# Kernel optimization log

Measured on AMD Instinct MI355X. Metric: run time of the kernel, lower is better.

Reference implementation:

```python
import jax, jax.numpy as jnp
import numpy as np

N_SPACE = 197  # spatial tokens (ViT-B/16: 196 patches + CLS)
T = 8          # frames, fixed by space_time_pos shape (197*8, dim)
H = 12         # heads


def setup_inputs() -> dict:
    key = jax.random.key(0)
    ks = jax.random.split(key, 8)
    dim = 768
    B = 8
    Nq = 1576
    scale = dim ** -0.5
    return {
        "s_x": jax.random.normal(ks[0], (N_SPACE, B * T, dim), jnp.float32),
        "t_x": jax.random.normal(ks[1], (B, Nq, dim), jnp.float32),
        "space_time_pos": scale * jax.random.normal(ks[2], (N_SPACE * T, dim), jnp.float32),
        "q_w": jax.random.normal(ks[3], (dim, dim), jnp.float32) * 0.02,
        "q_b": jnp.zeros((dim,), jnp.float32),
        "kv_w": jax.random.normal(ks[4], (2 * dim, dim), jnp.float32) * 0.02,
        "kv_b": jnp.zeros((2 * dim,), jnp.float32),
        "proj_w": jax.random.normal(ks[5], (dim, dim), jnp.float32) * 0.02,
        "proj_b": jnp.zeros((dim,), jnp.float32),
    }


def reference(s_x, t_x, space_time_pos, q_w, q_b, kv_w, kv_b, proj_w, proj_b):
    n, BT, dim = s_x.shape
    B, Nq, _ = t_x.shape
    t = BT // B
    head_dim = dim // H
    scale = head_dim ** -0.5

    # rearrange 'n (b t) d -> b (t n) d'
    s = s_x.reshape(n, B, t, dim).transpose(1, 2, 0, 3).reshape(B, t * n, dim)
    s = s + space_time_pos  # (B, t*n, dim)

    # Q from t_x, K/V from s
    q = t_x @ q_w.T + q_b                      # (B, Nq, dim)
    kv = s @ kv_w.T + kv_b                     # (B, t*n, 2*dim)
    Nk = t * n
    # 'b n (e h d) -> e b h n d'
    kv = kv.reshape(B, Nk, 2, H, head_dim).transpose(2, 0, 3, 1, 4)
    k, v = kv[0], kv[1]                        # (B, H, Nk, hd)
    q = q.reshape(B, Nq, H, head_dim).transpose(0, 2, 1, 3) * scale  # (B, H, Nq, hd)

    attn = jnp.einsum('bhqd,bhkd->bhqk', q, k)
    attn = jax.nn.softmax(attn, axis=-1)
    out = jnp.einsum('bhqk,bhkd->bhqd', attn, v)   # (B, H, Nq, hd)
    out = out.transpose(0, 2, 1, 3).reshape(B, Nq, dim)
    return out @ proj_w.T + proj_b
```

## Files before the change

kernel.cpp:

```cpp
#include <hip/hip_runtime.h>
#include <stdint.h>

#define NSPACE 197
#define TFRAMES 8
#define NH 12
#define DIM 768
#define HD 64
#define BATCH 8
#define NQ 1576
#define NK 1576
#define M_REAL 12608
#define M_PAD 12672
#define VT_LD 1600

typedef __attribute__((ext_vector_type(8))) short s16x8;
typedef __attribute__((ext_vector_type(4))) short s16x4;
typedef __attribute__((ext_vector_type(4))) float f32x4;

__device__ inline uint16_t f2bf(float f) {
    union { float f; uint32_t i; } c; c.f = f;
    uint32_t r = c.i + 0x7FFF + ((c.i >> 16) & 1);
    return (uint16_t)(r >> 16);
}
__device__ inline uint32_t pack2bf(float lo, float hi) {
    union { float f; uint32_t i; } a, b; a.f = lo; b.f = hi;
    return ((a.i + 0x8000u) >> 16) | ((b.i + 0x8000u) & 0xFFFF0000u);
}


__global__ void conv_f2b(const float* __restrict__ src, uint16_t* __restrict__ dst, int n8) {
    int chunk = blockIdx.x * 256 + threadIdx.x;
    if (chunk >= n8) return;
    size_t off = (size_t)chunk * 8;
    float4 a = *(const float4*)(src + off);
    float4 b = *(const float4*)(src + off + 4);
    s16x8 o;
    o[0] = (short)f2bf(a.x); o[1] = (short)f2bf(a.y);
    o[2] = (short)f2bf(a.z); o[3] = (short)f2bf(a.w);
    o[4] = (short)f2bf(b.x); o[5] = (short)f2bf(b.y);
    o[6] = (short)f2bf(b.z); o[7] = (short)f2bf(b.w);
    *(s16x8*)(dst + off) = o;
}

__global__ void fill_x(const float* __restrict__ t_x, uint16_t* __restrict__ x_pad) {
    int chunk = blockIdx.x * 256 + threadIdx.x;
    const int total = M_PAD * (DIM / 8);
    if (chunk >= total) return;
    size_t off = (size_t)chunk * 8;
    s16x8 o;
    if (off < (size_t)M_REAL * DIM) {
        float4 a = *(const float4*)(t_x + off);
        float4 b = *(const float4*)(t_x + off + 4);
        o[0] = (short)f2bf(a.x); o[1] = (short)f2bf(a.y);
        o[2] = (short)f2bf(a.z); o[3] = (short)f2bf(a.w);
        o[4] = (short)f2bf(b.x); o[5] = (short)f2bf(b.y);
        o[6] = (short)f2bf(b.z); o[7] = (short)f2bf(b.w);
    } else {
        for (int j = 0; j < 8; j++) o[j] = 0;
    }
    *(s16x8*)(x_pad + off) = o;
}

__global__ void fill_s(const float* __restrict__ s_x, const float* __restrict__ pos,
                       uint16_t* __restrict__ s_pad) {
    int chunk = blockIdx.x * 256 + threadIdx.x;
    const int total = M_PAD * (DIM / 8);
    if (chunk >= total) return;
    int i = chunk / (DIM / 8);
    int cc = chunk - i * (DIM / 8);
    int d0 = cc * 8;
    uint16_t* dst = s_pad + (size_t)i * DIM + d0;
    if (i >= M_REAL) {
        s16x8 z; for (int j = 0; j < 8; j++) z[j] = 0;
        *(s16x8*)dst = z;
        return;
    }
    int b = i / NK, rr = i - b * NK;
    int t_i = rr / NSPACE, n_i = rr - t_i * NSPACE;
    const float* src = s_x + ((size_t)(n_i * (BATCH * TFRAMES) + b * TFRAMES + t_i)) * DIM + d0;
    const float* ps = pos + (size_t)rr * DIM + d0;
    float4 a0 = *(const float4*)src;
    float4 a1 = *(const float4*)(src + 4);
    float4 p0 = *(const float4*)ps;
    float4 p1 = *(const float4*)(ps + 4);
    s16x8 o;
    o[0] = (short)f2bf(a0.x + p0.x); o[1] = (short)f2bf(a0.y + p0.y);
    o[2] = (short)f2bf(a0.z + p0.z); o[3] = (short)f2bf(a0.w + p0.w);
    o[4] = (short)f2bf(a1.x + p1.x); o[5] = (short)f2bf(a1.y + p1.y);
    o[6] = (short)f2bf(a1.z + p1.z); o[7] = (short)f2bf(a1.w + p1.w);
    *(s16x8*)dst = o;
}

template <int MODE>
__global__ __launch_bounds__(256)
void gemm_bt(const uint16_t* __restrict__ A, const uint16_t* __restrict__ W,
             const float* __restrict__ bias,
             uint16_t* __restrict__ out0, uint16_t* __restrict__ out1,
             float* __restrict__ outf) {
    __shared__ uint16_t As[128 * 40];
    __shared__ uint16_t Bs[128 * 40];
    const int t = threadIdx.x;
    const int lane = t & 63, w = t >> 6;
    const int r16 = lane & 15, quad = lane >> 4;
    const int wm = w >> 1, wn = w & 1;
    const int m0 = blockIdx.y * 128;
    const int n0 = blockIdx.x * 128;

    f32x4 acc[4][4];
    for (int a = 0; a < 4; a++)
        for (int bb = 0; bb < 4; bb++)
            for (int r = 0; r < 4; r++) acc[a][bb][r] = 0.f;

    for (int kk = 0; kk < DIM; kk += 32) {
        for (int i2 = 0; i2 < 2; i2++) {
            int c = t + i2 * 256;
            int row = c >> 2, kc = (c & 3) * 8;
            *(s16x8*)&As[row * 40 + kc] = *(const s16x8*)&A[(size_t)(m0 + row) * DIM + kk + kc];
            *(s16x8*)&Bs[row * 40 + kc] = *(const s16x8*)&W[(size_t)(n0 + row) * DIM + kk + kc];
        }
        __syncthreads();
        s16x8 af[4], bfr[4];
        for (int mt = 0; mt < 4; mt++)
            af[mt] = *(const s16x8*)&As[(wm * 64 + mt * 16 + r16) * 40 + quad * 8];
        for (int nt = 0; nt < 4; nt++)
            bfr[nt] = *(const s16x8*)&Bs[(wn * 64 + nt * 16 + r16) * 40 + quad * 8];
        for (int mt = 0; mt < 4; mt++)
            for (int nt = 0; nt < 4; nt++)
                acc[mt][nt] = __builtin_amdgcn_mfma_f32_16x16x32_bf16(af[mt], bfr[nt], acc[mt][nt], 0, 0, 0);
        __syncthreads();
    }

    for (int mt = 0; mt < 4; mt++)
        for (int nt = 0; nt < 4; nt++) {
            int col = n0 + wn * 64 + nt * 16 + r16;
            float bz = bias[col];
            int rowb = m0 + wm * 64 + mt * 16 + quad * 4;
            for (int r = 0; r < 4; r++) {
                int i = rowb + r;
                if (i >= M_REAL) continue;
                float v = acc[mt][nt][r] + bz;
                if (MODE == 0) {
                    int b = i / NQ, nq = i - b * NQ;
                    int h = col >> 6, d = col & 63;
                    out0[(size_t)(((b * NH + h) * NQ) + nq) * HD + d] = f2bf(v * 0.18033688011112042f);
                } else if (MODE == 1) {
                    int b = i / NK, nk = i - b * NK;
                    if (col < DIM) {
                        int h = col >> 6, d = col & 63;
                        out0[(size_t)(((b * NH + h) * NK) + nk) * HD + d] = f2bf(v);
                    } else {
                        int c2 = col - DIM;
                        int h = c2 >> 6, d = c2 & 63;
                        out1[(size_t)(((b * NH + h) * NK) + nk) * HD + d] = f2bf(v);
                    }
                } else {
                    outf[(size_t)i * DIM + col] = v;
                }
            }
        }
}

__global__ __launch_bounds__(256)
void transpose_v(const uint16_t* __restrict__ v, uint16_t* __restrict__ vt) {
    __shared__ uint16_t T[64 * 72];
    int tile = blockIdx.x, bh = blockIdx.y;
    int nk0 = tile * 64;
    const uint16_t* V = v + (size_t)bh * NK * HD;
    uint16_t* VT = vt + (size_t)bh * HD * VT_LD;
    int tid = threadIdx.x;
    int rr = tid >> 3;
    int c8 = (tid & 7) * 8;
    for (int p = 0; p < 2; p++) {
        int lr = p * 32 + rr;
        int nk = nk0 + lr;
        s16x8 val;
        if (nk < NK) val = *(const s16x8*)(V + (size_t)nk * HD + c8);
        else for (int j = 0; j < 8; j++) val[j] = 0;
        for (int j = 0; j < 8; j++)
            T[(c8 + j) * 72 + lr] = (uint16_t)val[j];
    }
    __syncthreads();
    for (int p = 0; p < 2; p++) {
        int d = p * 32 + rr;
        s16x8 o = *(const s16x8*)&T[d * 72 + c8];
        *(s16x8*)(VT + (size_t)d * VT_LD + nk0 + c8) = o;
    }
}

#define NITER 50
__global__ __launch_bounds__(256)
void flash_attn(const uint16_t* __restrict__ q_buf, const uint16_t* __restrict__ k_buf,
                const uint16_t* __restrict__ vt_buf, uint16_t* __restrict__ ao) {
    __shared__ uint16_t Kb[2][32 * 72];
    __shared__ uint16_t Vb[2][64 * 40];
    int h = blockIdx.y, b = blockIdx.z;
    int tid = threadIdx.x;
    int lane = tid & 63, w = tid >> 6;
    int r16 = lane & 15, quad = lane >> 4;
    size_t bh = (size_t)(b * NH + h);
    const uint16_t* Q = q_buf + bh * NQ * HD;
    const uint16_t* K = k_buf + bh * NK * HD;
    const uint16_t* VT = vt_buf + bh * HD * VT_LD;
    int q0 = blockIdx.x * 128 + w * 32;

    const int kg = tid >> 3;
    const int kc = (tid & 7) * 8;
    const int kslot = ((kg >> 3) << 2) + (kg & 3) + ((kg & 4) ? 16 : 0);
    const int vd = tid >> 2;
    const int vc = (tid & 3) * 8;
    const uint16_t* Kg = K + (size_t)kg * HD + kc;
    const uint16_t* Vg = VT + (size_t)vd * VT_LD + vc;
    uint16_t* Kw = &Kb[0][kslot * 72 + kc];
    uint16_t* Vw = &Vb[0][vd * 40 + vc];
    const int KBSZ = 32 * 72, VBSZ = 64 * 40;

    s16x8 qf[2][2];
    for (int m = 0; m < 2; m++) {
        int qrow = q0 + m * 16 + r16;
        if (qrow < NQ) {
            qf[m][0] = *(const s16x8*)(Q + (size_t)qrow * HD + quad * 8);
            qf[m][1] = *(const s16x8*)(Q + (size_t)qrow * HD + 32 + quad * 8);
        } else {
            for (int j = 0; j < 8; j++) { qf[m][0][j] = 0; qf[m][1][j] = 0; }
        }
    }

    f32x4 oT[2][4];
    f32x4 lsum4[2];
    for (int m = 0; m < 2; m++) {
        for (int dt = 0; dt < 4; dt++)
            for (int r = 0; r < 4; r++) oT[m][dt][r] = 0.f;
        for (int r = 0; r < 4; r++) lsum4[m][r] = 0.f;
    }

    {
        s16x8 kv = *(const s16x8*)Kg;
        s16x8 vv = *(const s16x8*)Vg;
        *(s16x8*)Kw = kv;
        *(s16x8*)Vw = vv;
    }
    __syncthreads();

    for (int it = 0; it < NITER; it++) {
        int kb = it * 32;
        int cur = it & 1, nxt = cur ^ 1;
        s16x8 knv, vnv;
        bool have_next = (it + 1 < NITER);
        if (have_next) {
            knv = *(const s16x8*)(Kg + (size_t)(kb + 32) * HD);
            vnv = *(const s16x8*)(Vg + kb + 32);
        }

        const uint16_t* Kc = &Kb[cur][0];
        const uint16_t* Vc = &Vb[cur][0];
        s16x8 kfA0 = *(const s16x8*)(Kc + r16 * 72 + quad * 8);
        s16x8 kfA1 = *(const s16x8*)(Kc + r16 * 72 + 32 + quad * 8);
        s16x8 kfB0 = *(const s16x8*)(Kc + (16 + r16) * 72 + quad * 8);
        s16x8 kfB1 = *(const s16x8*)(Kc + (16 + r16) * 72 + 32 + quad * 8);

        s16x8 pf[2];
        if (it < NITER - 1) {
            #pragma unroll
            for (int m = 0; m < 2; m++) {
                f32x4 sA, sB;
                for (int r = 0; r < 4; r++) { sA[r] = 0.f; sB[r] = 0.f; }
                sA = __builtin_amdgcn_mfma_f32_16x16x32_bf16(kfA0, qf[m][0], sA, 0, 0, 0);
                sA = __builtin_amdgcn_mfma_f32_16x16x32_bf16(kfA1, qf[m][1], sA, 0, 0, 0);
                sB = __builtin_amdgcn_mfma_f32_16x16x32_bf16(kfB0, qf[m][0], sB, 0, 0, 0);
                sB = __builtin_amdgcn_mfma_f32_16x16x32_bf16(kfB1, qf[m][1], sB, 0, 0, 0);
                f32x4 pA, pB;
                #pragma unroll
                for (int r = 0; r < 4; r++) { pA[r] = exp2f(sA[r]); pB[r] = exp2f(sB[r]); }
                lsum4[m] += pA;
                lsum4[m] += pB;
                union { s16x8 v; uint32_t u[4]; } pk;
                pk.u[0] = pack2bf(pA[0], pA[1]);
                pk.u[1] = pack2bf(pA[2], pA[3]);
                pk.u[2] = pack2bf(pB[0], pB[1]);
                pk.u[3] = pack2bf(pB[2], pB[3]);
                pf[m] = pk.v;
            }
        } else {
            #pragma unroll
            for (int m = 0; m < 2; m++) {
                f32x4 sA, sB;
                for (int r = 0; r < 4; r++) { sA[r] = 0.f; sB[r] = 0.f; }
                sA = __builtin_amdgcn_mfma_f32_16x16x32_bf16(kfA0, qf[m][0], sA, 0, 0, 0);
                sA = __builtin_amdgcn_mfma_f32_16x16x32_bf16(kfA1, qf[m][1], sA, 0, 0, 0);
                sB = __builtin_amdgcn_mfma_f32_16x16x32_bf16(kfB0, qf[m][0], sB, 0, 0, 0);
                sB = __builtin_amdgcn_mfma_f32_16x16x32_bf16(kfB1, qf[m][1], sB, 0, 0, 0);
                f32x4 pA, pB;
                #pragma unroll
                for (int r = 0; r < 4; r++) {
                    pA[r] = (kb + quad * 8 + r < NK)     ? exp2f(sA[r]) : 0.f;
                    pB[r] = (kb + quad * 8 + 4 + r < NK) ? exp2f(sB[r]) : 0.f;
                }
                lsum4[m] += pA;
                lsum4[m] += pB;
                union { s16x8 v; uint32_t u[4]; } pk;
                pk.u[0] = pack2bf(pA[0], pA[1]);
                pk.u[1] = pack2bf(pA[2], pA[3]);
                pk.u[2] = pack2bf(pB[0], pB[1]);
                pk.u[3] = pack2bf(pB[2], pB[3]);
                pf[m] = pk.v;
            }
        }
        #pragma unroll
        for (int dt = 0; dt < 4; dt++) {
            s16x8 vf = *(const s16x8*)(Vc + (dt * 16 + r16) * 40 + quad * 8);
            oT[0][dt] = __builtin_amdgcn_mfma_f32_16x16x32_bf16(vf, pf[0], oT[0][dt], 0, 0, 0);
            oT[1][dt] = __builtin_amdgcn_mfma_f32_16x16x32_bf16(vf, pf[1], oT[1][dt], 0, 0, 0);
        }
        if (have_next) {
            *(s16x8*)(Kw + nxt * KBSZ) = knv;
            *(s16x8*)(Vw + nxt * VBSZ) = vnv;
        }
        __syncthreads();
    }

    #pragma unroll
    for (int m = 0; m < 2; m++) {
        float rs = lsum4[m][0] + lsum4[m][1] + lsum4[m][2] + lsum4[m][3];
        rs += __shfl_xor(rs, 16);
        rs += __shfl_xor(rs, 32);
        int q = q0 + m * 16 + r16;
        if (q >= NQ) continue;
        float inv = 1.0f / rs;
        size_t rowoff = (size_t)(b * NQ + q) * DIM + h * HD;
        #pragma unroll
        for (int dt = 0; dt < 4; dt++) {
            s16x4 o4;
            o4[0] = (short)f2bf(oT[m][dt][0] * inv);
            o4[1] = (short)f2bf(oT[m][dt][1] * inv);
            o4[2] = (short)f2bf(oT[m][dt][2] * inv);
            o4[3] = (short)f2bf(oT[m][dt][3] * inv);
            *(s16x4*)(ao + rowoff + dt * 16 + quad * 4) = o4;
        }
    }
}

extern "C" void kernel_launch(void* const* d_in, const int* in_sizes, int n_in,
                              void* d_out, int out_size, void* d_ws, size_t ws_size,
                              hipStream_t stream) {
    const float* s_x    = (const float*)d_in[0];
    const float* t_x    = (const float*)d_in[1];
    const float* pos    = (const float*)d_in[2];
    const float* q_w    = (const float*)d_in[3];
    const float* q_b    = (const float*)d_in[4];
    const float* kv_w   = (const float*)d_in[5];
    const float* kv_b   = (const float*)d_in[6];
    const float* proj_w = (const float*)d_in[7];
    const float* proj_b = (const float*)d_in[8];
    float* out = (float*)d_out;

    char* ws = (char*)d_ws;
    size_t off = 0;
    auto carve = [&](size_t bytes) {
        void* p = ws + off;
        off += (bytes + 255) & ~(size_t)255;
        return p;
    };
    uint16_t* x_pad  = (uint16_t*)carve((size_t)M_PAD * DIM * 2);
    uint16_t* s_pad  = (uint16_t*)carve((size_t)M_PAD * DIM * 2);
    uint16_t* q_buf  = (uint16_t*)carve((size_t)BATCH * NH * NQ * HD * 2);
    uint16_t* k_buf  = (uint16_t*)carve((size_t)BATCH * NH * NK * HD * 2);
    uint16_t* vt_buf = (uint16_t*)carve((size_t)BATCH * NH * HD * VT_LD * 2);
    uint16_t* wbuf   = (uint16_t*)carve((size_t)2 * DIM * DIM * 2);
    if (off > ws_size) return;
    uint16_t* v_buf = x_pad;
    uint16_t* ao    = x_pad;

    const int fill_blocks = (M_PAD * (DIM / 8) + 255) / 256;
    const int wq8 = DIM * DIM / 8, wkv8 = 2 * DIM * DIM / 8;

    fill_x<<<fill_blocks, 256, 0, stream>>>(t_x, x_pad);
    fill_s<<<fill_blocks, 256, 0, stream>>>(s_x, pos, s_pad);

    conv_f2b<<<(wq8 + 255) / 256, 256, 0, stream>>>(q_w, wbuf, wq8);
    gemm_bt<0><<<dim3(DIM / 128, M_PAD / 128), 256, 0, stream>>>(x_pad, wbuf, q_b, q_buf, nullptr, nullptr);

    conv_f2b<<<(wkv8 + 255) / 256, 256, 0, stream>>>(kv_w, wbuf, wkv8);
    gemm_bt<1><<<dim3(2 * DIM / 128, M_PAD / 128), 256, 0, stream>>>(s_pad, wbuf, kv_b, k_buf, v_buf, nullptr);
    transpose_v<<<dim3(VT_LD / 64, BATCH * NH), 256, 0, stream>>>(v_buf, vt_buf);

    flash_attn<<<dim3((NQ + 127) / 128, NH, BATCH), 256, 0, stream>>>(q_buf, k_buf, vt_buf, ao);

    conv_f2b<<<(wq8 + 255) / 256, 256, 0, stream>>>(proj_w, wbuf, wq8);
    gemm_bt<2><<<dim3(DIM / 128, M_PAD / 128), 256, 0, stream>>>(ao, wbuf, proj_b, nullptr, nullptr, out);
}
```

Before: 440.6 us.

## Use direct global-to-LDS loads in GEMM and hardware bf16 pack conversion

The GEMM tile staging now uses global_load_lds to copy A and W tiles straight into shared memory instead of going through registers, and the shared tiles drop their padding from a row stride of 40 to 32. Every float-to-bf16 conversion in the fill kernels, the softmax probability pack and the attention output is replaced with the hardware v_cvt_pk_bf16_f32 instruction. The aim is to cut VGPR traffic and ALU work on conversions and loads. Removing the padding brings back LDS bank conflicts on the fragment reads, and loads are still not double-buffered.

```diff
diff --git a/kernel.cpp b/kernel.cpp
--- a/kernel.cpp
+++ b/kernel.cpp
@@ -22,9 +22,18 @@
     uint32_t r = c.i + 0x7FFF + ((c.i >> 16) & 1);
     return (uint16_t)(r >> 16);
 }
-__device__ inline uint32_t pack2bf(float lo, float hi) {
-    union { float f; uint32_t i; } a, b; a.f = lo; b.f = hi;
-    return ((a.i + 0x8000u) >> 16) | ((b.i + 0x8000u) & 0xFFFF0000u);
+
+__device__ inline uint32_t cvtpk_bf16(float lo, float hi) {
+    uint32_t r;
+    asm("v_cvt_pk_bf16_f32 %0, %1, %2" : "=v"(r) : "v"(lo), "v"(hi));
+    return r;
+}
+
+__device__ inline void gld_lds16(const uint16_t* g, uint16_t* l) {
+    __builtin_amdgcn_global_load_lds(
+        (const __attribute__((address_space(1))) void*)g,
+        (__attribute__((address_space(3))) void*)l,
+        16, 0, 0);
 }
 
 
@@ -34,12 +43,12 @@
     size_t off = (size_t)chunk * 8;
     float4 a = *(const float4*)(src + off);
     float4 b = *(const float4*)(src + off + 4);
-    s16x8 o;
-    o[0] = (short)f2bf(a.x); o[1] = (short)f2bf(a.y);
-    o[2] = (short)f2bf(a.z); o[3] = (short)f2bf(a.w);
-    o[4] = (short)f2bf(b.x); o[5] = (short)f2bf(b.y);
-    o[6] = (short)f2bf(b.z); o[7] = (short)f2bf(b.w);
-    *(s16x8*)(dst + off) = o;
+    union { s16x8 v; uint32_t u[4]; } o;
+    o.u[0] = cvtpk_bf16(a.x, a.y);
+    o.u[1] = cvtpk_bf16(a.z, a.w);
+    o.u[2] = cvtpk_bf16(b.x, b.y);
+    o.u[3] = cvtpk_bf16(b.z, b.w);
+    *(s16x8*)(dst + off) = o.v;
 }
 
 __global__ void fill_x(const float* __restrict__ t_x, uint16_t* __restrict__ x_pad) {
@@ -51,10 +60,12 @@
     if (off < (size_t)M_REAL * DIM) {
         float4 a = *(const float4*)(t_x + off);
         float4 b = *(const float4*)(t_x + off + 4);
-        o[0] = (short)f2bf(a.x); o[1] = (short)f2bf(a.y);
-        o[2] = (short)f2bf(a.z); o[3] = (short)f2bf(a.w);
-        o[4] = (short)f2bf(b.x); o[5] = (short)f2bf(b.y);
-        o[6] = (short)f2bf(b.z); o[7] = (short)f2bf(b.w);
+        union { s16x8 v; uint32_t u[4]; } p;
+        p.u[0] = cvtpk_bf16(a.x, a.y);
+        p.u[1] = cvtpk_bf16(a.z, a.w);
+        p.u[2] = cvtpk_bf16(b.x, b.y);
+        p.u[3] = cvtpk_bf16(b.z, b.w);
+        o = p.v;
     } else {
         for (int j = 0; j < 8; j++) o[j] = 0;
     }
@@ -83,12 +94,12 @@
     float4 a1 = *(const float4*)(src + 4);
     float4 p0 = *(const float4*)ps;
     float4 p1 = *(const float4*)(ps + 4);
-    s16x8 o;
-    o[0] = (short)f2bf(a0.x + p0.x); o[1] = (short)f2bf(a0.y + p0.y);
-    o[2] = (short)f2bf(a0.z + p0.z); o[3] = (short)f2bf(a0.w + p0.w);
-    o[4] = (short)f2bf(a1.x + p1.x); o[5] = (short)f2bf(a1.y + p1.y);
-    o[6] = (short)f2bf(a1.z + p1.z); o[7] = (short)f2bf(a1.w + p1.w);
-    *(s16x8*)dst = o;
+    union { s16x8 v; uint32_t u[4]; } o;
+    o.u[0] = cvtpk_bf16(a0.x + p0.x, a0.y + p0.y);
+    o.u[1] = cvtpk_bf16(a0.z + p0.z, a0.w + p0.w);
+    o.u[2] = cvtpk_bf16(a1.x + p1.x, a1.y + p1.y);
+    o.u[3] = cvtpk_bf16(a1.z + p1.z, a1.w + p1.w);
+    *(s16x8*)dst = o.v;
 }
 
 template <int MODE>
@@ -97,8 +108,8 @@
              const float* __restrict__ bias,
              uint16_t* __restrict__ out0, uint16_t* __restrict__ out1,
              float* __restrict__ outf) {
-    __shared__ uint16_t As[128 * 40];
-    __shared__ uint16_t Bs[128 * 40];
+    __shared__ uint16_t As[128 * 32];
+    __shared__ uint16_t Bs[128 * 32];
     const int t = threadIdx.x;
     const int lane = t & 63, w = t >> 6;
     const int r16 = lane & 15, quad = lane >> 4;
@@ -106,24 +117,29 @@
     const int m0 = blockIdx.y * 128;
     const int n0 = blockIdx.x * 128;
 
+    const int srow = w * 32 + (lane >> 2);
+    const int scol = (lane & 3) * 8;
+    const uint16_t* Ag = A + (size_t)(m0 + srow) * DIM + scol;
+    const uint16_t* Wg = W + (size_t)(n0 + srow) * DIM + scol;
+    uint16_t* Asw = &As[w * 32 * 32];
+    uint16_t* Bsw = &Bs[w * 32 * 32];
+
     f32x4 acc[4][4];
     for (int a = 0; a < 4; a++)
         for (int bb = 0; bb < 4; bb++)
             for (int r = 0; r < 4; r++) acc[a][bb][r] = 0.f;
 
     for (int kk = 0; kk < DIM; kk += 32) {
-        for (int i2 = 0; i2 < 2; i2++) {
-            int c = t + i2 * 256;
-            int row = c >> 2, kc = (c & 3) * 8;
-            *(s16x8*)&As[row * 40 + kc] = *(const s16x8*)&A[(size_t)(m0 + row) * DIM + kk + kc];
-            *(s16x8*)&Bs[row * 40 + kc] = *(const s16x8*)&W[(size_t)(n0 + row) * DIM + kk + kc];
-        }
+        gld_lds16(Ag + kk, Asw);
+        gld_lds16(Ag + kk + (size_t)16 * DIM, Asw + 16 * 32);
+        gld_lds16(Wg + kk, Bsw);
+        gld_lds16(Wg + kk + (size_t)16 * DIM, Bsw + 16 * 32);
         __syncthreads();
         s16x8 af[4], bfr[4];
         for (int mt = 0; mt < 4; mt++)
-            af[mt] = *(const s16x8*)&As[(wm * 64 + mt * 16 + r16) * 40 + quad * 8];
+            af[mt] = *(const s16x8*)&As[(wm * 64 + mt * 16 + r16) * 32 + quad * 8];
         for (int nt = 0; nt < 4; nt++)
-            bfr[nt] = *(const s16x8*)&Bs[(wn * 64 + nt * 16 + r16) * 40 + quad * 8];
+            bfr[nt] = *(const s16x8*)&Bs[(wn * 64 + nt * 16 + r16) * 32 + quad * 8];
         for (int mt = 0; mt < 4; mt++)
             for (int nt = 0; nt < 4; nt++)
                 acc[mt][nt] = __builtin_amdgcn_mfma_f32_16x16x32_bf16(af[mt], bfr[nt], acc[mt][nt], 0, 0, 0);
@@ -274,10 +290,10 @@
                 lsum4[m] += pA;
                 lsum4[m] += pB;
                 union { s16x8 v; uint32_t u[4]; } pk;
-                pk.u[0] = pack2bf(pA[0], pA[1]);
-                pk.u[1] = pack2bf(pA[2], pA[3]);
-                pk.u[2] = pack2bf(pB[0], pB[1]);
-                pk.u[3] = pack2bf(pB[2], pB[3]);
+                pk.u[0] = cvtpk_bf16(pA[0], pA[1]);
+                pk.u[1] = cvtpk_bf16(pA[2], pA[3]);
+                pk.u[2] = cvtpk_bf16(pB[0], pB[1]);
+                pk.u[3] = cvtpk_bf16(pB[2], pB[3]);
                 pf[m] = pk.v;
             }
         } else {
@@ -298,10 +314,10 @@
                 lsum4[m] += pA;
                 lsum4[m] += pB;
                 union { s16x8 v; uint32_t u[4]; } pk;
-                pk.u[0] = pack2bf(pA[0], pA[1]);
-                pk.u[1] = pack2bf(pA[2], pA[3]);
-                pk.u[2] = pack2bf(pB[0], pB[1]);
-                pk.u[3] = pack2bf(pB[2], pB[3]);
+                pk.u[0] = cvtpk_bf16(pA[0], pA[1]);
+                pk.u[1] = cvtpk_bf16(pA[2], pA[3]);
+                pk.u[2] = cvtpk_bf16(pB[0], pB[1]);
+                pk.u[3] = cvtpk_bf16(pB[2], pB[3]);
                 pf[m] = pk.v;
             }
         }
@@ -329,12 +345,10 @@
         size_t rowoff = (size_t)(b * NQ + q) * DIM + h * HD;
         #pragma unroll
         for (int dt = 0; dt < 4; dt++) {
-            s16x4 o4;
-            o4[0] = (short)f2bf(oT[m][dt][0] * inv);
-            o4[1] = (short)f2bf(oT[m][dt][1] * inv);
-            o4[2] = (short)f2bf(oT[m][dt][2] * inv);
-            o4[3] = (short)f2bf(oT[m][dt][3] * inv);
-            *(s16x4*)(ao + rowoff + dt * 16 + quad * 4) = o4;
+            union { s16x4 v; uint32_t u[2]; } o;
+            o.u[0] = cvtpk_bf16(oT[m][dt][0] * inv, oT[m][dt][1] * inv);
+            o.u[1] = cvtpk_bf16(oT[m][dt][2] * inv, oT[m][dt][3] * inv);
+            *(s16x4*)(ao + rowoff + dt * 16 + quad * 4) = o.v;
         }
     }
 }
```

Result: faster. 390.4 us (-11.4%).
